# Performance work log

Measured on AMD Instinct MI355X. Metric: run time of the kernel, lower is better.

The kernel has to match this reference:

```python
import jax, jax.numpy as jnp
import numpy as np

# Kobayashi dendrite-growth parameters (init_params values from the repo)
TAU = 3e-4
EPSILONB = 0.01
KAPPA = 1.8
DELTA = 0.02
ANISO = 6.0
ALPHA = 0.9
GAMMA = 10.0
TEQ = 1.0
THETA0 = 0.2
PIX = 4.0 * np.arctan(1.0)  # pi
DX = 0.03
DY = 0.03
DT = 1e-4

B, H, W = 4, 2048, 2048


def lap(u, dx, dy):
    # 5-point Laplacian, periodic boundaries. x = last axis, y = second-to-last.
    return ((jnp.roll(u, -1, -1) + jnp.roll(u, 1, -1) - 2.0 * u) / (dx * dx)
            + (jnp.roll(u, -1, -2) + jnp.roll(u, 1, -2) - 2.0 * u) / (dy * dy))


def grad(u, axis_name, d):
    ax = -1 if axis_name == 'x' else -2
    return (jnp.roll(u, -1, ax) - jnp.roll(u, 1, ax)) / (2.0 * d)


def setup_inputs() -> dict:
    key = jax.random.key(0)
    k1, k2 = jax.random.split(key)
    phi = jax.random.uniform(k1, (B, H, W), dtype=jnp.float32)
    tempr = jax.random.uniform(k2, (B, H, W), dtype=jnp.float32)
    return {"phi": phi, "tempr": tempr}


def reference(phi, tempr):
    lap_phi = lap(phi, DX, DY)
    lap_tempr = lap(tempr, DX, DY)
    phidx = grad(phi, 'x', DX)
    phidy = grad(phi, 'y', DY)
    theta = jnp.arctan2(phidy, phidx)
    epsilon = EPSILONB * (1.0 + DELTA * jnp.cos(ANISO * (theta - THETA0)))
    epsilon_deriv = -EPSILONB * ANISO * DELTA * jnp.sin(ANISO * (theta - THETA0))
    prod_mat1 = epsilon * epsilon_deriv * phidx
    prod_mat2 = -epsilon * epsilon_deriv * phidy
    term1 = grad(prod_mat1, 'y', DY)
    term2 = grad(prod_mat2, 'x', DX)
    m = ALPHA / PIX * jnp.arctan(GAMMA * (TEQ - tempr))
    dphi_dt = DT / TAU * (term1 + term2 + epsilon ** 2 * lap_phi
                          + phi * (1.0 - phi) * (phi - 0.5 + m))
    phi_new = phi + dphi_dt
    tempr_new = tempr + DT * lap_tempr + KAPPA * dphi_dt
    return (phi_new, tempr_new)
```

## Files before the change

kernel.cpp:

```cpp
#include <hip/hip_runtime.h>
#include <math.h>


#define Bz 4
#define Hd 2048
#define Wd 2048
#define TX 64
#define TY 32
#define PW (TX + 4)
#define PH (TY + 4)
#define QW (TX + 2)
#define QH (TY + 2)

#define INV2D   16.6666666666667f
#define INVD2   1111.11111111111f
#define DT_TAU  0.333333333333333f
#define DTc     1e-4f
#define KAPPAc  1.8f
#define EPSB    0.01f
#define DELTAc  0.02f
#define ANISOc  6.0f
#define A_PI    0.2864788975654116f
#define GAMMAc  10.0f
#define TEQc    1.0f
#define C6T0    0.3623577544766736f
#define S6T0    0.9320390859672263f

__global__ __launch_bounds__(256) void dendrite_step(
    const float* __restrict__ phi, const float* __restrict__ tempr,
    float* __restrict__ out_phi, float* __restrict__ out_tempr)
{
    __shared__ float sphi[PH * PW];
    __shared__ float sp1[QH * QW];
    __shared__ float sp2[QH * QW];
    __shared__ float se2[QH * QW];

    const int tid = threadIdx.x;
    const int x0 = blockIdx.x * TX;
    const int y0 = blockIdx.y * TY;
    const int base = blockIdx.z * (Hd * Wd);

    for (int i = tid; i < PH * PW; i += 256) {
        int r = i / PW;
        int c = i - r * PW;
        int gy = (y0 + r - 2) & (Hd - 1);
        int gx = (x0 + c - 2) & (Wd - 1);
        sphi[i] = phi[base + gy * Wd + gx];
    }
    __syncthreads();

    for (int i = tid; i < QH * QW; i += 256) {
        int r = i / QW;
        int c = i - r * QW;
        int p = (r + 1) * PW + (c + 1);
        float phidx = (sphi[p + 1]  - sphi[p - 1])  * INV2D;
        float phidy = (sphi[p + PW] - sphi[p - PW]) * INV2D;

        float r2 = phidx * phidx + phidy * phidy;
        float rinv = (r2 > 0.0f) ? rsqrtf(r2) : 0.0f;
        float ct = (r2 > 0.0f) ? phidx * rinv : 1.0f;
        float st = phidy * rinv;

        float c2 = ct * ct - st * st;
        float s2 = 2.0f * ct * st;
        float c4 = c2 * c2 - s2 * s2;
        float s4 = 2.0f * c2 * s2;
        float c6 = c4 * c2 - s4 * s2;
        float s6 = s4 * c2 + c4 * s2;

        float cosA = c6 * C6T0 + s6 * S6T0;
        float sinA = s6 * C6T0 - c6 * S6T0;

        float eps  = EPSB * (1.0f + DELTAc * cosA);
        float epsd = -EPSB * ANISOc * DELTAc * sinA;
        float ee   = eps * epsd;

        sp1[i] = ee * phidx;
        sp2[i] = -ee * phidy;
        se2[i] = eps * eps;
    }
    __syncthreads();

    const int tx = tid & 63;
    const int ty0 = tid >> 6;

    for (int k = 0; k < TY / 4; ++k) {
        int y = ty0 + k * 4;
        int q = (y + 1) * QW + (tx + 1);
        int p = (y + 2) * PW + (tx + 2);

        float term1 = (sp1[q + QW] - sp1[q - QW]) * INV2D;
        float term2 = (sp2[q + 1]  - sp2[q - 1])  * INV2D;

        float phic = sphi[p];
        float lap_phi = (sphi[p + 1] + sphi[p - 1] - 2.0f * phic) * INVD2
                      + (sphi[p + PW] + sphi[p - PW] - 2.0f * phic) * INVD2;

        int gy = y0 + y;
        int gx = x0 + tx;
        int gxp = (gx + 1) & (Wd - 1);
        int gxm = (gx - 1) & (Wd - 1);
        int gyp = (gy + 1) & (Hd - 1);
        int gym = (gy - 1) & (Hd - 1);
        int rowb = base + gy * Wd;

        float tc = tempr[rowb + gx];
        float lap_t = (tempr[rowb + gxp] + tempr[rowb + gxm] - 2.0f * tc) * INVD2
                    + (tempr[base + gyp * Wd + gx] + tempr[base + gym * Wd + gx]
                       - 2.0f * tc) * INVD2;

        float m = A_PI * atanf(GAMMAc * (TEQc - tc));
        float dphi = DT_TAU * (term1 + term2 + se2[q] * lap_phi
                               + phic * (1.0f - phic) * (phic - 0.5f + m));

        int gidx = rowb + gx;
        out_phi[gidx] = phic + dphi;
        out_tempr[gidx] = tc + DTc * lap_t + KAPPAc * dphi;
    }
}

extern "C" void kernel_launch(void* const* d_in, const int* in_sizes, int n_in,
                              void* d_out, int out_size, void* d_ws, size_t ws_size,
                              hipStream_t stream) {
    const float* phi = (const float*)d_in[0];
    const float* tempr = (const float*)d_in[1];
    float* out_phi = (float*)d_out;
    float* out_tempr = out_phi + (size_t)Bz * Hd * Wd;

    dim3 grid(Wd / TX, Hd / TY, Bz);
    dendrite_step<<<grid, 256, 0, stream>>>(phi, tempr, out_phi, out_tempr);
}
```

Baseline: 285.9 us.

## Store stencil tiles in fp16 shared memory and roll rows through registers

Shared-memory copies of phi and of the flux products (with eps squared) are now packed as __half2, with the flux products scaled by 4096 before storage. The phi tile is loaded with float2 reads, and each gradient thread now handles two columns. The final stage gives each thread 8 consecutive rows and keeps the vertical stencil neighbours of phi, the flux term and tempr in registers across iterations, which removes repeated global and LDS reads. Launch bounds now ask for 8 blocks per CU. The aim is to cut LDS footprint and traffic, at the cost of fp16 rounding, including on the centre phi value that goes straight into the output, which could break accuracy tolerances.

Measured after the change: 245.7 us. 1.16x faster.

```diff
diff --git a/kernel.cpp b/kernel.cpp
--- a/kernel.cpp
+++ b/kernel.cpp
@@ -1,4 +1,5 @@
 #include <hip/hip_runtime.h>
+#include <hip/hip_fp16.h>
 #include <math.h>
 
 
@@ -7,10 +8,10 @@
 #define Wd 2048
 #define TX 64
 #define TY 32
-#define PW (TX + 4)
-#define PH (TY + 4)
-#define QW (TX + 2)
-#define QH (TY + 2)
+#define PW 68
+#define PH 36
+#define QW 66
+#define QH 34
 
 #define INV2D   16.6666666666667f
 #define INVD2   1111.11111111111f
@@ -25,97 +26,147 @@
 #define TEQc    1.0f
 #define C6T0    0.3623577544766736f
 #define S6T0    0.9320390859672263f
+#define SC      4096.0f
+#define ISC     (1.0f/4096.0f)
 
-__global__ __launch_bounds__(256) void dendrite_step(
+__device__ __forceinline__ void prod_chain(float phidx, float phidy,
+                                           float& sp1s, float& sp2s, float& se2s)
+{
+    float r2 = phidx * phidx + phidy * phidy;
+    float rinv = (r2 > 0.0f) ? rsqrtf(r2) : 0.0f;
+    float ct = (r2 > 0.0f) ? phidx * rinv : 1.0f;
+    float st = phidy * rinv;
+    float c2 = ct * ct - st * st;
+    float s2 = 2.0f * ct * st;
+    float c4 = c2 * c2 - s2 * s2;
+    float s4 = 2.0f * c2 * s2;
+    float c6 = c4 * c2 - s4 * s2;
+    float s6 = s4 * c2 + c4 * s2;
+    float cosA = c6 * C6T0 + s6 * S6T0;
+    float sinA = s6 * C6T0 - c6 * S6T0;
+    float eps  = EPSB * (1.0f + DELTAc * cosA);
+    float epsd = -EPSB * ANISOc * DELTAc * sinA;
+    float eesc = eps * epsd * SC;
+    sp1s = eesc * phidx;
+    sp2s = -eesc * phidy;
+    se2s = eps * eps * SC;
+}
+
+__global__ __launch_bounds__(256, 8) void dendrite_step(
     const float* __restrict__ phi, const float* __restrict__ tempr,
     float* __restrict__ out_phi, float* __restrict__ out_tempr)
 {
-    __shared__ float sphi[PH * PW];
-    __shared__ float sp1[QH * QW];
-    __shared__ float sp2[QH * QW];
-    __shared__ float se2[QH * QW];
+    __shared__ __half2 sphi2[PH * PW / 2];
+    __shared__ __half2 spk[QH * QW];
+    __shared__ __half2 se2_2[QH * QW / 2];
 
     const int tid = threadIdx.x;
     const int x0 = blockIdx.x * TX;
     const int y0 = blockIdx.y * TY;
     const int base = blockIdx.z * (Hd * Wd);
 
-    for (int i = tid; i < PH * PW; i += 256) {
-        int r = i / PW;
-        int c = i - r * PW;
+    for (int i = tid; i < PH * PW / 2; i += 256) {
+        int r = i / (PW / 2);
+        int c2 = i - r * (PW / 2);
         int gy = (y0 + r - 2) & (Hd - 1);
-        int gx = (x0 + c - 2) & (Wd - 1);
-        sphi[i] = phi[base + gy * Wd + gx];
+        int gx = (x0 + 2 * c2 - 2) & (Wd - 1);
+        float2 v = *(const float2*)(phi + base + gy * Wd + gx);
+        sphi2[i] = __floats2half2_rn(v.x, v.y);
     }
     __syncthreads();
 
-    for (int i = tid; i < QH * QW; i += 256) {
-        int r = i / QW;
-        int c = i - r * QW;
-        int p = (r + 1) * PW + (c + 1);
-        float phidx = (sphi[p + 1]  - sphi[p - 1])  * INV2D;
-        float phidy = (sphi[p + PW] - sphi[p - PW]) * INV2D;
+    const __half* sph = (const __half*)sphi2;
+    for (int i = tid; i < QH * (QW / 2); i += 256) {
+        int r = i / (QW / 2);
+        int c2 = i - r * (QW / 2);
+        int cQ = 2 * c2;
+        int pr = r + 1;
+        int rowc = pr * (PW / 2) + c2;
+        __half2 A = sphi2[rowc];
+        __half2 Bv = sphi2[rowc + 1];
+        __half2 U0 = sphi2[rowc - PW / 2];
+        __half2 U1 = sphi2[rowc - PW / 2 + 1];
+        __half2 D0 = sphi2[rowc + PW / 2];
+        __half2 D1 = sphi2[rowc + PW / 2 + 1];
 
-        float r2 = phidx * phidx + phidy * phidy;
-        float rinv = (r2 > 0.0f) ? rsqrtf(r2) : 0.0f;
-        float ct = (r2 > 0.0f) ? phidx * rinv : 1.0f;
-        float st = phidy * rinv;
+        float f0 = __low2float(A),  f1 = __high2float(A);
+        float f2 = __low2float(Bv), f3 = __high2float(Bv);
 
-        float c2 = ct * ct - st * st;
-        float s2 = 2.0f * ct * st;
-        float c4 = c2 * c2 - s2 * s2;
-        float s4 = 2.0f * c2 * s2;
-        float c6 = c4 * c2 - s4 * s2;
-        float s6 = s4 * c2 + c4 * s2;
+        float sp1a, sp2a, se2a, sp1b, sp2b, se2b;
+        prod_chain((f2 - f0) * INV2D,
+                   (__high2float(D0) - __high2float(U0)) * INV2D,
+                   sp1a, sp2a, se2a);
+        prod_chain((f3 - f1) * INV2D,
+                   (__low2float(D1) - __low2float(U1)) * INV2D,
+                   sp1b, sp2b, se2b);
 
-        float cosA = c6 * C6T0 + s6 * S6T0;
-        float sinA = s6 * C6T0 - c6 * S6T0;
-
-        float eps  = EPSB * (1.0f + DELTAc * cosA);
-        float epsd = -EPSB * ANISOc * DELTAc * sinA;
-        float ee   = eps * epsd;
-
-        sp1[i] = ee * phidx;
-        sp2[i] = -ee * phidy;
-        se2[i] = eps * eps;
+        int q = r * QW + cQ;
+        spk[q]     = __floats2half2_rn(sp1a, sp2a);
+        spk[q + 1] = __floats2half2_rn(sp1b, sp2b);
+        se2_2[r * (QW / 2) + c2] = __floats2half2_rn(se2a, se2b);
     }
     __syncthreads();
 
+    const __half* se2h = (const __half*)se2_2;
     const int tx = tid & 63;
-    const int ty0 = tid >> 6;
+    const int tg = tid >> 6;
+    const int ys = tg * 8;
+    const int col = tx + 2;
+    const int gx = x0 + tx;
+    const int gxm = (gx - 1) & (Wd - 1);
+    const int gxp = (gx + 1) & (Wd - 1);
 
-    for (int k = 0; k < TY / 4; ++k) {
-        int y = ty0 + k * 4;
-        int q = (y + 1) * QW + (tx + 1);
-        int p = (y + 2) * PW + (tx + 2);
+    float pm = __half2float(sph[(ys + 1) * PW + col]);
+    float pc_ = __half2float(sph[(ys + 2) * PW + col]);
+    float s1m = __low2float(spk[ys * QW + tx + 1]);
+    float s1c = __low2float(spk[(ys + 1) * QW + tx + 1]);
+    float tm  = tempr[base + ((y0 + ys - 1) & (Hd - 1)) * Wd + gx];
+    {
+        int rb = base + (y0 + ys) * Wd;
+        (void)rb;
+    }
+    int rb0 = base + (y0 + ys) * Wd;
+    float tcl = tempr[rb0 + gxm];
+    float tcc = tempr[rb0 + gx];
+    float tcr = tempr[rb0 + gxp];
 
-        float term1 = (sp1[q + QW] - sp1[q - QW]) * INV2D;
-        float term2 = (sp2[q + 1]  - sp2[q - 1])  * INV2D;
+    for (int k = 0; k < 8; ++k) {
+        int y = ys + k;
+        int qrow = y + 1;
+        int prow = y + 2;
 
-        float phic = sphi[p];
-        float lap_phi = (sphi[p + 1] + sphi[p - 1] - 2.0f * phic) * INVD2
-                      + (sphi[p + PW] + sphi[p - PW] - 2.0f * phic) * INVD2;
+        float pp = __half2float(sph[(prow + 1) * PW + col]);
+        float pl = __half2float(sph[prow * PW + col - 1]);
+        float prr = __half2float(sph[prow * PW + col + 1]);
+        float lap_phi = (pl + prr - 2.0f * pc_) * INVD2
+                      + (pm + pp - 2.0f * pc_) * INVD2;
 
-        int gy = y0 + y;
-        int gx = x0 + tx;
-        int gxp = (gx + 1) & (Wd - 1);
-        int gxm = (gx - 1) & (Wd - 1);
-        int gyp = (gy + 1) & (Hd - 1);
-        int gym = (gy - 1) & (Hd - 1);
-        int rowb = base + gy * Wd;
+        float s1p = __low2float(spk[(qrow + 1) * QW + tx + 1]);
+        float term1 = (s1p - s1m) * (INV2D * ISC);
+        float sp2l = __high2float(spk[qrow * QW + tx]);
+        float sp2r = __high2float(spk[qrow * QW + tx + 2]);
+        float term2 = (sp2r - sp2l) * (INV2D * ISC);
+        float e2 = __half2float(se2h[qrow * QW + tx + 1]) * ISC;
 
-        float tc = tempr[rowb + gx];
-        float lap_t = (tempr[rowb + gxp] + tempr[rowb + gxm] - 2.0f * tc) * INVD2
-                    + (tempr[base + gyp * Wd + gx] + tempr[base + gym * Wd + gx]
-                       - 2.0f * tc) * INVD2;
+        int rbp = base + ((y0 + y + 1) & (Hd - 1)) * Wd;
+        float tpl = tempr[rbp + gxm];
+        float tpc = tempr[rbp + gx];
+        float tpr = tempr[rbp + gxp];
 
-        float m = A_PI * atanf(GAMMAc * (TEQc - tc));
-        float dphi = DT_TAU * (term1 + term2 + se2[q] * lap_phi
-                               + phic * (1.0f - phic) * (phic - 0.5f + m));
+        float lap_t = (tcl + tcr - 2.0f * tcc) * INVD2
+                    + (tm + tpc - 2.0f * tcc) * INVD2;
 
-        int gidx = rowb + gx;
-        out_phi[gidx] = phic + dphi;
-        out_tempr[gidx] = tc + DTc * lap_t + KAPPAc * dphi;
+        float m = A_PI * atanf(GAMMAc * (TEQc - tcc));
+        float dphi = DT_TAU * (term1 + term2 + e2 * lap_phi
+                               + pc_ * (1.0f - pc_) * (pc_ - 0.5f + m));
+
+        int gidx = base + (y0 + y) * Wd + gx;
+        out_phi[gidx] = pc_ + dphi;
+        out_tempr[gidx] = tcc + DTc * lap_t + KAPPAc * dphi;
+
+        pm = pc_; pc_ = pp;
+        s1m = s1c; s1c = s1p;
+        tm = tcc; tcl = tpl; tcc = tpc; tcr = tpr;
     }
 }
 
```
